# Kernel optimization log

Hardware: AMD Instinct MI355X
Metric: run time of the kernel (lower is better)

## Reference

```python
import jax, jax.numpy as jnp
import numpy as np

B, C, F, T, D = 8, 128, 256, 128, 32


def setup_inputs() -> dict:
    key = jax.random.key(0)
    ks = jax.random.split(key, 7)
    x = jax.random.normal(ks[0], (B, C, F, T), jnp.float32)
    # 1x1 Conv2d over the T axis == linear map on T; weights [out, T], bias [out]
    Wk = jax.random.normal(ks[1], (D, T), jnp.float32) * 0.05
    bk = jax.random.normal(ks[2], (D,), jnp.float32) * 0.05
    Wq = jax.random.normal(ks[3], (D, T), jnp.float32) * 0.05
    bq = jax.random.normal(ks[4], (D,), jnp.float32) * 0.05
    Wv = jax.random.normal(ks[5], (T, T), jnp.float32) * 0.05
    bv = jax.random.normal(ks[6], (T,), jnp.float32) * 0.05
    return {"x": x, "Wk": Wk, "bk": bk, "Wq": Wq, "bq": bq, "Wv": Wv, "bv": bv}


def _proj(xp, W, b):
    # xp: [B, C2, F, T]; W: [out, T] -> [B, F, out, C2]
    return jnp.einsum('bcft,dt->bfdc', xp, W) + b[None, None, :, None]


def reference(x, Wk, bk, Wq, bq, Wv, bv):
    C2 = x.shape[1] // 2
    xr, xi = x[:, :C2], x[:, C2:]
    k_r = _proj(xr, Wk, bk)  # [B,F,D,C2]
    k_i = _proj(xi, Wk, bk)
    q_r = _proj(xr, Wq, bq)
    q_i = _proj(xi, Wq, bq)
    v_r = _proj(xr, Wv, bv)  # [B,F,T,C2]
    v_i = _proj(xi, Wv, bv)
    # complex P = k^H... actually plain k^T q (no conjugate in source)
    P_r = jnp.einsum('bfdc,bfde->bfce', k_r, q_r) - jnp.einsum('bfdc,bfde->bfce', k_i, q_i)
    P_i = jnp.einsum('bfdc,bfde->bfce', k_r, q_i) + jnp.einsum('bfdc,bfde->bfce', k_i, q_r)
    # independent softmaxes over dim=2 (the first C2 axis)
    W_r = jax.nn.softmax(P_r, axis=2)
    W_i = jax.nn.softmax(P_i, axis=2)
    # output = v @ W (complex)
    o_r = jnp.einsum('bftc,bfce->bfte', v_r, W_r) - jnp.einsum('bftc,bfce->bfte', v_i, W_i)
    o_i = jnp.einsum('bftc,bfce->bfte', v_r, W_i) + jnp.einsum('bftc,bfce->bfte', v_i, W_r)
    # permute [B,F,T,C2] -> [B,C2,F,T], concat real/imag on channel axis
    o_r = jnp.transpose(o_r, (0, 3, 1, 2))
    o_i = jnp.transpose(o_i, (0, 3, 1, 2))
    return jnp.concatenate([o_r, o_i], axis=1)  # [B,C,F,T]
```

## Files before the change

kernel.cpp:

```cpp
#include <hip/hip_runtime.h>

typedef __attribute__((ext_vector_type(8))) __bf16 bf16x8;
typedef __attribute__((ext_vector_type(8))) unsigned short ushort8;
typedef __attribute__((ext_vector_type(4))) unsigned short ushort4v;
typedef __attribute__((ext_vector_type(4))) float f32x4;

namespace {
constexpr int kB = 8, kC = 128, kF = 256, kT = 128;

__device__ __forceinline__ int addrXT(int t, int p) { return t * 128 + (p ^ ((t & 7) << 3)); }
__device__ __forceinline__ int addrU(int ri, int e, int s) { return ri * 8192 + e * 128 + (s ^ ((e & 7) << 3)); }
__device__ __forceinline__ int addrK(int m, int c, int p) { return 16384 + m * 2048 + c * 32 + (p ^ ((c & 3) << 3)); }

__device__ __forceinline__ unsigned short b16(float f) {
    __bf16 h = (__bf16)f;
    return __builtin_bit_cast(unsigned short, h);
}

__device__ __forceinline__ bf16x8 ldfrag(const unsigned short* lds, int idx) {
    return __builtin_bit_cast(bf16x8, *(const ushort8*)(lds + idx));
}

__device__ __forceinline__ bf16x8 fneg(bf16x8 a) {
    ushort8 u = __builtin_bit_cast(ushort8, a);
    u ^= (unsigned short)0x8000;
    return __builtin_bit_cast(bf16x8, u);
}

__device__ __forceinline__ bf16x8 fragWg(const float* p) {
    f32x4 a = *(const f32x4*)p;
    f32x4 c = *(const f32x4*)(p + 4);
    bf16x8 r;
    r[0] = (__bf16)a[0]; r[1] = (__bf16)a[1]; r[2] = (__bf16)a[2]; r[3] = (__bf16)a[3];
    r[4] = (__bf16)c[0]; r[5] = (__bf16)c[1]; r[6] = (__bf16)c[2]; r[7] = (__bf16)c[3];
    return r;
}
}

__global__ __launch_bounds__(256, 4)
void chanattn_mfma2(const float* __restrict__ x,
                    const float* __restrict__ Wk, const float* __restrict__ bk,
                    const float* __restrict__ Wq, const float* __restrict__ bq,
                    const float* __restrict__ Wv, const float* __restrict__ bv,
                    float* __restrict__ out)
{
    __shared__ __align__(16) unsigned short lds[20480];

    const int f = blockIdx.x, b = blockIdx.y;
    const int tid = threadIdx.x;
    const int lane = tid & 63;
    const int w = tid >> 6;
    const int lr = lane & 15;
    const int lg = lane >> 4;
    const size_t cstr = (size_t)kF * kT;
    const float* xb = x + ((size_t)b * kC * kF + f) * kT;

    bf16x8 bqr, bqi;
    {
        bf16x8 xr_f[4], xi_f[4];
        #pragma unroll
        for (int ks = 0; ks < 4; ++ks) {
            xr_f[ks] = fragWg(xb + (size_t)(16 * w + lr) * cstr + ks * 32 + 8 * lg);
            xi_f[ks] = fragWg(xb + (size_t)(64 + 16 * w + lr) * cstr + ks * 32 + 8 * lg);
        }
        f32x4 qacc[2][2], kacc[2][2];
        #pragma unroll
        for (int ri = 0; ri < 2; ++ri)
            #pragma unroll
            for (int dt = 0; dt < 2; ++dt) {
                qacc[ri][dt] = (f32x4){0.f, 0.f, 0.f, 0.f};
                kacc[ri][dt] = (f32x4){0.f, 0.f, 0.f, 0.f};
            }
        #pragma unroll
        for (int dt = 0; dt < 2; ++dt)
            #pragma unroll
            for (int ks = 0; ks < 4; ++ks) {
                bf16x8 wq = fragWg(Wq + (size_t)(16 * dt + lr) * kT + ks * 32 + 8 * lg);
                bf16x8 wk = fragWg(Wk + (size_t)(16 * dt + lr) * kT + ks * 32 + 8 * lg);
                qacc[0][dt] = __builtin_amdgcn_mfma_f32_16x16x32_bf16(wq, xr_f[ks], qacc[0][dt], 0, 0, 0);
                qacc[1][dt] = __builtin_amdgcn_mfma_f32_16x16x32_bf16(wq, xi_f[ks], qacc[1][dt], 0, 0, 0);
                kacc[0][dt] = __builtin_amdgcn_mfma_f32_16x16x32_bf16(xr_f[ks], wk, kacc[0][dt], 0, 0, 0);
                kacc[1][dt] = __builtin_amdgcn_mfma_f32_16x16x32_bf16(xi_f[ks], wk, kacc[1][dt], 0, 0, 0);
            }
        const float bk0 = bk[lr], bk1 = bk[16 + lr];
        #pragma unroll
        for (int dt = 0; dt < 2; ++dt) {
            const int pcol = 8 * ((lr >> 2) & 3) + 4 * dt + (lr & 3);
            const float bb = dt ? bk1 : bk0;
            #pragma unroll
            for (int r = 0; r < 4; ++r) {
                const int c = 16 * w + 4 * lg + r;
                lds[addrK(0, c, pcol)] = b16(kacc[0][dt][r] + bb);
                lds[addrK(1, c, pcol)] = b16(kacc[1][dt][r] + bb);
            }
        }
        #pragma unroll
        for (int j = 0; j < 8; ++j) {
            const int dt = j >> 2, r = j & 3;
            const float bb = bq[16 * dt + 4 * lg + r];
            bqr[j] = (__bf16)(qacc[0][dt][r] + bb);
            bqi[j] = (__bf16)(qacc[1][dt][r] + bb);
        }
    }

    {
        const int c0 = 4 * (tid & 31);
        const int t0 = 4 * (tid >> 5);
        const int h  = c0 >> 6;
        const int cc = c0 & 63;
        const int p0 = 64 * h + 32 * (cc >> 5) + 8 * ((cc >> 2) & 3) + 4 * ((cc >> 4) & 1);
        #pragma unroll
        for (int tp = 0; tp < 4; ++tp) {
            const int t = t0 + 32 * tp;
            f32x4 v[4];
            #pragma unroll
            for (int j = 0; j < 4; ++j)
                v[j] = *(const f32x4*)(xb + (size_t)(c0 + j) * cstr + t);
            #pragma unroll
            for (int i = 0; i < 4; ++i) {
                ushort4v pk;
                pk[0] = b16(v[0][i]); pk[1] = b16(v[1][i]);
                pk[2] = b16(v[2][i]); pk[3] = b16(v[3][i]);
                *(ushort4v*)&lds[addrXT(t + i, p0)] = pk;
            }
        }
    }
    __syncthreads();

    f32x4 pr[4], pi[4];
    float inv_r, inv_i;
    {
        const f32x4 zero = {0.f, 0.f, 0.f, 0.f};
        #pragma unroll
        for (int ct = 0; ct < 4; ++ct) {
            bf16x8 akr = ldfrag(lds, addrK(0, ct * 16 + lr, 8 * lg));
            bf16x8 aki = ldfrag(lds, addrK(1, ct * 16 + lr, 8 * lg));
            pr[ct] = __builtin_amdgcn_mfma_f32_16x16x32_bf16(akr, bqr, zero, 0, 0, 0);
            pr[ct] = __builtin_amdgcn_mfma_f32_16x16x32_bf16(fneg(aki), bqi, pr[ct], 0, 0, 0);
            pi[ct] = __builtin_amdgcn_mfma_f32_16x16x32_bf16(akr, bqi, zero, 0, 0, 0);
            pi[ct] = __builtin_amdgcn_mfma_f32_16x16x32_bf16(aki, bqr, pi[ct], 0, 0, 0);
        }
        float mr = -1e30f, mi = -1e30f;
        #pragma unroll
        for (int ct = 0; ct < 4; ++ct)
            #pragma unroll
            for (int r = 0; r < 4; ++r) { mr = fmaxf(mr, pr[ct][r]); mi = fmaxf(mi, pi[ct][r]); }
        mr = fmaxf(mr, __shfl_xor(mr, 16)); mr = fmaxf(mr, __shfl_xor(mr, 32));
        mi = fmaxf(mi, __shfl_xor(mi, 16)); mi = fmaxf(mi, __shfl_xor(mi, 32));
        float sr = 0.f, si = 0.f;
        #pragma unroll
        for (int ct = 0; ct < 4; ++ct)
            #pragma unroll
            for (int r = 0; r < 4; ++r) {
                float er = __expf(pr[ct][r] - mr); pr[ct][r] = er; sr += er;
                float ei = __expf(pi[ct][r] - mi); pi[ct][r] = ei; si += ei;
            }
        sr += __shfl_xor(sr, 16); sr += __shfl_xor(sr, 32);
        si += __shfl_xor(si, 16); si += __shfl_xor(si, 32);
        inv_r = 1.f / sr; inv_i = 1.f / si;
    }

    bf16x8 awr[2], awi[2], awin[2];
    #pragma unroll
    for (int ks = 0; ks < 2; ++ks) {
        #pragma unroll
        for (int j = 0; j < 8; ++j) {
            const int ct = 2 * ks + (j >> 2), r = j & 3;
            awr[ks][j] = (__bf16)(pr[ct][r] * inv_r);
            awi[ks][j] = (__bf16)(pi[ct][r] * inv_i);
        }
        awin[ks] = fneg(awi[ks]);
    }

    f32x4 uacc_r[8], uacc_i[8];
    #pragma unroll
    for (int nt = 0; nt < 8; ++nt) {
        f32x4 ur = {0.f, 0.f, 0.f, 0.f}, ui = {0.f, 0.f, 0.f, 0.f};
        #pragma unroll
        for (int ks = 0; ks < 2; ++ks) {
            bf16x8 bxr = ldfrag(lds, addrXT(nt * 16 + lr, ks * 32 + 8 * lg));
            bf16x8 bxi = ldfrag(lds, addrXT(nt * 16 + lr, 64 + ks * 32 + 8 * lg));
            ur = __builtin_amdgcn_mfma_f32_16x16x32_bf16(awr[ks], bxr, ur, 0, 0, 0);
            ur = __builtin_amdgcn_mfma_f32_16x16x32_bf16(awin[ks], bxi, ur, 0, 0, 0);
            ui = __builtin_amdgcn_mfma_f32_16x16x32_bf16(awi[ks], bxr, ui, 0, 0, 0);
            ui = __builtin_amdgcn_mfma_f32_16x16x32_bf16(awr[ks], bxi, ui, 0, 0, 0);
        }
        uacc_r[nt] = ur; uacc_i[nt] = ui;
    }
    __syncthreads();
    #pragma unroll
    for (int nt = 0; nt < 8; ++nt)
        #pragma unroll
        for (int r = 0; r < 4; ++r) {
            const int e = 16 * w + 4 * lg + r;
            lds[addrU(0, e, nt * 16 + lr)] = b16(uacc_r[nt][r]);
            lds[addrU(1, e, nt * 16 + lr)] = b16(uacc_i[nt][r]);
        }
    __syncthreads();

    {
        #pragma unroll
        for (int mi_ = 0; mi_ < 2; ++mi_) {
            const int mt = 2 * w + mi_;
            bf16x8 av[4];
            #pragma unroll
            for (int ks = 0; ks < 4; ++ks)
                av[ks] = fragWg(Wv + (size_t)(mt * 16 + lr) * kT + ks * 32 + 8 * lg);
            float bvv[4];
            #pragma unroll
            for (int r = 0; r < 4; ++r) bvv[r] = 2.f * bv[mt * 16 + 4 * lg + r];

            #pragma unroll
            for (int et = 0; et < 4; ++et) {
                f32x4 aor = {0.f, 0.f, 0.f, 0.f}, aoi = {0.f, 0.f, 0.f, 0.f};
                #pragma unroll
                for (int ks = 0; ks < 4; ++ks) {
                    bf16x8 bur = ldfrag(lds, addrU(0, et * 16 + lr, ks * 32 + 8 * lg));
                    bf16x8 bui = ldfrag(lds, addrU(1, et * 16 + lr, ks * 32 + 8 * lg));
                    aor = __builtin_amdgcn_mfma_f32_16x16x32_bf16(av[ks], bur, aor, 0, 0, 0);
                    aoi = __builtin_amdgcn_mfma_f32_16x16x32_bf16(av[ks], bui, aoi, 0, 0, 0);
                }
                const int e = et * 16 + lr;
                const int tp0 = mt * 16 + 4 * lg;
                f32x4 vi;
                #pragma unroll
                for (int r = 0; r < 4; ++r) vi[r] = aoi[r] + bvv[r];
                *(f32x4*)(out + (((size_t)b * kC + e) * kF + f) * kT + tp0)      = aor;
                *(f32x4*)(out + (((size_t)b * kC + 64 + e) * kF + f) * kT + tp0) = vi;
            }
        }
    }
}

extern "C" void kernel_launch(void* const* d_in, const int* in_sizes, int n_in,
                              void* d_out, int out_size, void* d_ws, size_t ws_size,
                              hipStream_t stream) {
    const float* x  = (const float*)d_in[0];
    const float* Wk = (const float*)d_in[1];
    const float* bk = (const float*)d_in[2];
    const float* Wq = (const float*)d_in[3];
    const float* bq = (const float*)d_in[4];
    const float* Wv = (const float*)d_in[5];
    const float* bv = (const float*)d_in[6];
    float* out = (float*)d_out;

    dim3 grid(kF, kB);
    dim3 block(256);
    chanattn_mfma2<<<grid, block, 0, stream>>>(x, Wk, bk, Wq, bq, Wv, bv, out);
}
```

Before: 97.59 us.

## Process two frequency bins per block with register prefetch of next x tile

Each block now handles two consecutive f values in a loop, and the grid is halved. The x tile is loaded in halves into registers and the next bin's first half is prefetched while the current bin is being staged, so global load latency overlaps compute. The Q/K projection now reloads its x fragments inside the ks loop instead of holding them all at once, which lowers register pressure. In exchange the grid has fewer blocks, which may cut occupancy and parallelism, and an extra barrier is added per iteration.

```diff
diff --git a/kernel.cpp b/kernel.cpp
--- a/kernel.cpp
+++ b/kernel.cpp
@@ -17,8 +17,8 @@
     return __builtin_bit_cast(unsigned short, h);
 }
 
-__device__ __forceinline__ bf16x8 ldfrag(const unsigned short* lds, int idx) {
-    return __builtin_bit_cast(bf16x8, *(const ushort8*)(lds + idx));
+__device__ __forceinline__ bf16x8 ldfrag(const unsigned short* p, int idx) {
+    return __builtin_bit_cast(bf16x8, *(const ushort8*)(p + idx));
 }
 
 __device__ __forceinline__ bf16x8 fneg(bf16x8 a) {
@@ -38,197 +38,231 @@
 }
 
 __global__ __launch_bounds__(256, 4)
-void chanattn_mfma2(const float* __restrict__ x,
-                    const float* __restrict__ Wk, const float* __restrict__ bk,
-                    const float* __restrict__ Wq, const float* __restrict__ bq,
-                    const float* __restrict__ Wv, const float* __restrict__ bv,
-                    float* __restrict__ out)
+void chanattn_pipe(const float* __restrict__ x,
+                   const float* __restrict__ Wk, const float* __restrict__ bk,
+                   const float* __restrict__ Wq, const float* __restrict__ bq,
+                   const float* __restrict__ Wv, const float* __restrict__ bv,
+                   float* __restrict__ out)
 {
     __shared__ __align__(16) unsigned short lds[20480];
 
-    const int f = blockIdx.x, b = blockIdx.y;
+    const int bx = blockIdx.x, b = blockIdx.y;
     const int tid = threadIdx.x;
     const int lane = tid & 63;
     const int w = tid >> 6;
     const int lr = lane & 15;
     const int lg = lane >> 4;
     const size_t cstr = (size_t)kF * kT;
-    const float* xb = x + ((size_t)b * kC * kF + f) * kT;
-
-    bf16x8 bqr, bqi;
-    {
-        bf16x8 xr_f[4], xi_f[4];
-        #pragma unroll
-        for (int ks = 0; ks < 4; ++ks) {
-            xr_f[ks] = fragWg(xb + (size_t)(16 * w + lr) * cstr + ks * 32 + 8 * lg);
-            xi_f[ks] = fragWg(xb + (size_t)(64 + 16 * w + lr) * cstr + ks * 32 + 8 * lg);
-        }
-        f32x4 qacc[2][2], kacc[2][2];
-        #pragma unroll
-        for (int ri = 0; ri < 2; ++ri)
-            #pragma unroll
-            for (int dt = 0; dt < 2; ++dt) {
-                qacc[ri][dt] = (f32x4){0.f, 0.f, 0.f, 0.f};
-                kacc[ri][dt] = (f32x4){0.f, 0.f, 0.f, 0.f};
-            }
-        #pragma unroll
-        for (int dt = 0; dt < 2; ++dt)
-            #pragma unroll
-            for (int ks = 0; ks < 4; ++ks) {
-                bf16x8 wq = fragWg(Wq + (size_t)(16 * dt + lr) * kT + ks * 32 + 8 * lg);
-                bf16x8 wk = fragWg(Wk + (size_t)(16 * dt + lr) * kT + ks * 32 + 8 * lg);
-                qacc[0][dt] = __builtin_amdgcn_mfma_f32_16x16x32_bf16(wq, xr_f[ks], qacc[0][dt], 0, 0, 0);
-                qacc[1][dt] = __builtin_amdgcn_mfma_f32_16x16x32_bf16(wq, xi_f[ks], qacc[1][dt], 0, 0, 0);
-                kacc[0][dt] = __builtin_amdgcn_mfma_f32_16x16x32_bf16(xr_f[ks], wk, kacc[0][dt], 0, 0, 0);
-                kacc[1][dt] = __builtin_amdgcn_mfma_f32_16x16x32_bf16(xi_f[ks], wk, kacc[1][dt], 0, 0, 0);
-            }
-        const float bk0 = bk[lr], bk1 = bk[16 + lr];
-        #pragma unroll
-        for (int dt = 0; dt < 2; ++dt) {
-            const int pcol = 8 * ((lr >> 2) & 3) + 4 * dt + (lr & 3);
-            const float bb = dt ? bk1 : bk0;
-            #pragma unroll
-            for (int r = 0; r < 4; ++r) {
-                const int c = 16 * w + 4 * lg + r;
-                lds[addrK(0, c, pcol)] = b16(kacc[0][dt][r] + bb);
-                lds[addrK(1, c, pcol)] = b16(kacc[1][dt][r] + bb);
-            }
-        }
-        #pragma unroll
-        for (int j = 0; j < 8; ++j) {
-            const int dt = j >> 2, r = j & 3;
-            const float bb = bq[16 * dt + 4 * lg + r];
-            bqr[j] = (__bf16)(qacc[0][dt][r] + bb);
-            bqi[j] = (__bf16)(qacc[1][dt][r] + bb);
-        }
-    }
-
-    {
-        const int c0 = 4 * (tid & 31);
-        const int t0 = 4 * (tid >> 5);
-        const int h  = c0 >> 6;
-        const int cc = c0 & 63;
-        const int p0 = 64 * h + 32 * (cc >> 5) + 8 * ((cc >> 2) & 3) + 4 * ((cc >> 4) & 1);
-        #pragma unroll
-        for (int tp = 0; tp < 4; ++tp) {
+
+    const int c0 = 4 * (tid & 31);
+    const int t0 = 4 * (tid >> 5);
+    const int h  = c0 >> 6;
+    const int cc = c0 & 63;
+    const int p0 = 64 * h + 32 * (cc >> 5) + 8 * ((cc >> 2) & 3) + 4 * ((cc >> 4) & 1);
+
+    const float* xb_base = x + ((size_t)b * kC * kF + 2 * bx) * kT;
+
+    f32x4 ph0[2][4], ph1[2][4];
+    #pragma unroll
+    for (int tp = 0; tp < 2; ++tp)
+        #pragma unroll
+        for (int j = 0; j < 4; ++j)
+            ph0[tp][j] = *(const f32x4*)(xb_base + (size_t)(c0 + j) * cstr + t0 + 32 * tp);
+
+    #pragma unroll 1
+    for (int n = 0; n < 2; ++n) {
+        const int f = 2 * bx + n;
+        const float* xb = x + ((size_t)b * kC * kF + f) * kT;
+
+        #pragma unroll
+        for (int tp = 0; tp < 2; ++tp)
+            #pragma unroll
+            for (int j = 0; j < 4; ++j)
+                ph1[tp][j] = *(const f32x4*)(xb + (size_t)(c0 + j) * cstr + t0 + 64 + 32 * tp);
+
+        #pragma unroll
+        for (int tp = 0; tp < 2; ++tp) {
             const int t = t0 + 32 * tp;
-            f32x4 v[4];
-            #pragma unroll
-            for (int j = 0; j < 4; ++j)
-                v[j] = *(const f32x4*)(xb + (size_t)(c0 + j) * cstr + t);
             #pragma unroll
             for (int i = 0; i < 4; ++i) {
                 ushort4v pk;
-                pk[0] = b16(v[0][i]); pk[1] = b16(v[1][i]);
-                pk[2] = b16(v[2][i]); pk[3] = b16(v[3][i]);
+                pk[0] = b16(ph0[tp][0][i]); pk[1] = b16(ph0[tp][1][i]);
+                pk[2] = b16(ph0[tp][2][i]); pk[3] = b16(ph0[tp][3][i]);
                 *(ushort4v*)&lds[addrXT(t + i, p0)] = pk;
             }
         }
-    }
-    __syncthreads();
-
-    f32x4 pr[4], pi[4];
-    float inv_r, inv_i;
-    {
-        const f32x4 zero = {0.f, 0.f, 0.f, 0.f};
-        #pragma unroll
-        for (int ct = 0; ct < 4; ++ct) {
-            bf16x8 akr = ldfrag(lds, addrK(0, ct * 16 + lr, 8 * lg));
-            bf16x8 aki = ldfrag(lds, addrK(1, ct * 16 + lr, 8 * lg));
-            pr[ct] = __builtin_amdgcn_mfma_f32_16x16x32_bf16(akr, bqr, zero, 0, 0, 0);
-            pr[ct] = __builtin_amdgcn_mfma_f32_16x16x32_bf16(fneg(aki), bqi, pr[ct], 0, 0, 0);
-            pi[ct] = __builtin_amdgcn_mfma_f32_16x16x32_bf16(akr, bqi, zero, 0, 0, 0);
-            pi[ct] = __builtin_amdgcn_mfma_f32_16x16x32_bf16(aki, bqr, pi[ct], 0, 0, 0);
-        }
-        float mr = -1e30f, mi = -1e30f;
-        #pragma unroll
-        for (int ct = 0; ct < 4; ++ct)
-            #pragma unroll
-            for (int r = 0; r < 4; ++r) { mr = fmaxf(mr, pr[ct][r]); mi = fmaxf(mi, pi[ct][r]); }
-        mr = fmaxf(mr, __shfl_xor(mr, 16)); mr = fmaxf(mr, __shfl_xor(mr, 32));
-        mi = fmaxf(mi, __shfl_xor(mi, 16)); mi = fmaxf(mi, __shfl_xor(mi, 32));
-        float sr = 0.f, si = 0.f;
-        #pragma unroll
-        for (int ct = 0; ct < 4; ++ct)
+
+        if (n == 0) {
+            const float* xb1 = xb_base + kT;
+            #pragma unroll
+            for (int tp = 0; tp < 2; ++tp)
+                #pragma unroll
+                for (int j = 0; j < 4; ++j)
+                    ph0[tp][j] = *(const f32x4*)(xb1 + (size_t)(c0 + j) * cstr + t0 + 32 * tp);
+        }
+
+        #pragma unroll
+        for (int tp = 0; tp < 2; ++tp) {
+            const int t = t0 + 64 + 32 * tp;
+            #pragma unroll
+            for (int i = 0; i < 4; ++i) {
+                ushort4v pk;
+                pk[0] = b16(ph1[tp][0][i]); pk[1] = b16(ph1[tp][1][i]);
+                pk[2] = b16(ph1[tp][2][i]); pk[3] = b16(ph1[tp][3][i]);
+                *(ushort4v*)&lds[addrXT(t + i, p0)] = pk;
+            }
+        }
+
+        bf16x8 bqr, bqi;
+        {
+            f32x4 qacc[2][2], kacc[2][2];
+            #pragma unroll
+            for (int ri = 0; ri < 2; ++ri)
+                #pragma unroll
+                for (int dt = 0; dt < 2; ++dt) {
+                    qacc[ri][dt] = (f32x4){0.f, 0.f, 0.f, 0.f};
+                    kacc[ri][dt] = (f32x4){0.f, 0.f, 0.f, 0.f};
+                }
+            #pragma unroll
+            for (int ks = 0; ks < 4; ++ks) {
+                bf16x8 xr_f = fragWg(xb + (size_t)(16 * w + lr) * cstr + ks * 32 + 8 * lg);
+                bf16x8 xi_f = fragWg(xb + (size_t)(64 + 16 * w + lr) * cstr + ks * 32 + 8 * lg);
+                #pragma unroll
+                for (int dt = 0; dt < 2; ++dt) {
+                    bf16x8 wq = fragWg(Wq + (size_t)(16 * dt + lr) * kT + ks * 32 + 8 * lg);
+                    bf16x8 wk = fragWg(Wk + (size_t)(16 * dt + lr) * kT + ks * 32 + 8 * lg);
+                    qacc[0][dt] = __builtin_amdgcn_mfma_f32_16x16x32_bf16(wq, xr_f, qacc[0][dt], 0, 0, 0);
+                    qacc[1][dt] = __builtin_amdgcn_mfma_f32_16x16x32_bf16(wq, xi_f, qacc[1][dt], 0, 0, 0);
+                    kacc[0][dt] = __builtin_amdgcn_mfma_f32_16x16x32_bf16(xr_f, wk, kacc[0][dt], 0, 0, 0);
+                    kacc[1][dt] = __builtin_amdgcn_mfma_f32_16x16x32_bf16(xi_f, wk, kacc[1][dt], 0, 0, 0);
+                }
+            }
+            const float bk0 = bk[lr], bk1 = bk[16 + lr];
+            #pragma unroll
+            for (int dt = 0; dt < 2; ++dt) {
+                const int pcol = 8 * ((lr >> 2) & 3) + 4 * dt + (lr & 3);
+                const float bb = dt ? bk1 : bk0;
+                #pragma unroll
+                for (int r = 0; r < 4; ++r) {
+                    const int c = 16 * w + 4 * lg + r;
+                    lds[addrK(0, c, pcol)] = b16(kacc[0][dt][r] + bb);
+                    lds[addrK(1, c, pcol)] = b16(kacc[1][dt][r] + bb);
+                }
+            }
+            #pragma unroll
+            for (int j = 0; j < 8; ++j) {
+                const int dt = j >> 2, r = j & 3;
+                const float bb = bq[16 * dt + 4 * lg + r];
+                bqr[j] = (__bf16)(qacc[0][dt][r] + bb);
+                bqi[j] = (__bf16)(qacc[1][dt][r] + bb);
+            }
+        }
+        __syncthreads();
+
+        f32x4 pr[4], pi[4];
+        float inv_r, inv_i;
+        {
+            const f32x4 zero = {0.f, 0.f, 0.f, 0.f};
+            #pragma unroll
+            for (int ct = 0; ct < 4; ++ct) {
+                bf16x8 akr = ldfrag(lds, addrK(0, ct * 16 + lr, 8 * lg));
+                bf16x8 aki = ldfrag(lds, addrK(1, ct * 16 + lr, 8 * lg));
+                pr[ct] = __builtin_amdgcn_mfma_f32_16x16x32_bf16(akr, bqr, zero, 0, 0, 0);
+                pr[ct] = __builtin_amdgcn_mfma_f32_16x16x32_bf16(fneg(aki), bqi, pr[ct], 0, 0, 0);
+                pi[ct] = __builtin_amdgcn_mfma_f32_16x16x32_bf16(akr, bqi, zero, 0, 0, 0);
+                pi[ct] = __builtin_amdgcn_mfma_f32_16x16x32_bf16(aki, bqr, pi[ct], 0, 0, 0);
+            }
+            float mr = -1e30f, mi = -1e30f;
+            #pragma unroll
+            for (int ct = 0; ct < 4; ++ct)
+                #pragma unroll
+                for (int r = 0; r < 4; ++r) { mr = fmaxf(mr, pr[ct][r]); mi = fmaxf(mi, pi[ct][r]); }
+            mr = fmaxf(mr, __shfl_xor(mr, 16)); mr = fmaxf(mr, __shfl_xor(mr, 32));
+            mi = fmaxf(mi, __shfl_xor(mi, 16)); mi = fmaxf(mi, __shfl_xor(mi, 32));
+            float sr = 0.f, si = 0.f;
+            #pragma unroll
+            for (int ct = 0; ct < 4; ++ct)
+                #pragma unroll
+                for (int r = 0; r < 4; ++r) {
+                    float er = __expf(pr[ct][r] - mr); pr[ct][r] = er; sr += er;
+                    float ei = __expf(pi[ct][r] - mi); pi[ct][r] = ei; si += ei;
+                }
+            sr += __shfl_xor(sr, 16); sr += __shfl_xor(sr, 32);
+            si += __shfl_xor(si, 16); si += __shfl_xor(si, 32);
+            inv_r = 1.f / sr; inv_i = 1.f / si;
+        }
+
+        bf16x8 awr[2], awi[2], awin[2];
+        #pragma unroll
+        for (int ks = 0; ks < 2; ++ks) {
+            #pragma unroll
+            for (int j = 0; j < 8; ++j) {
+                const int ct = 2 * ks + (j >> 2), r = j & 3;
+                awr[ks][j] = (__bf16)(pr[ct][r] * inv_r);
+                awi[ks][j] = (__bf16)(pi[ct][r] * inv_i);
+            }
+            awin[ks] = fneg(awi[ks]);
+        }
+
+        f32x4 uacc_r[8], uacc_i[8];
+        #pragma unroll
+        for (int nt = 0; nt < 8; ++nt) {
+            f32x4 ur = {0.f, 0.f, 0.f, 0.f}, ui = {0.f, 0.f, 0.f, 0.f};
+            #pragma unroll
+            for (int ks = 0; ks < 2; ++ks) {
+                bf16x8 bxr = ldfrag(lds, addrXT(nt * 16 + lr, ks * 32 + 8 * lg));
+                bf16x8 bxi = ldfrag(lds, addrXT(nt * 16 + lr, 64 + ks * 32 + 8 * lg));
+                ur = __builtin_amdgcn_mfma_f32_16x16x32_bf16(awr[ks], bxr, ur, 0, 0, 0);
+                ur = __builtin_amdgcn_mfma_f32_16x16x32_bf16(awin[ks], bxi, ur, 0, 0, 0);
+                ui = __builtin_amdgcn_mfma_f32_16x16x32_bf16(awi[ks], bxr, ui, 0, 0, 0);
+                ui = __builtin_amdgcn_mfma_f32_16x16x32_bf16(awr[ks], bxi, ui, 0, 0, 0);
+            }
+            uacc_r[nt] = ur; uacc_i[nt] = ui;
+        }
+        __syncthreads();
+        #pragma unroll
+        for (int nt = 0; nt < 8; ++nt)
             #pragma unroll
             for (int r = 0; r < 4; ++r) {
-                float er = __expf(pr[ct][r] - mr); pr[ct][r] = er; sr += er;
-                float ei = __expf(pi[ct][r] - mi); pi[ct][r] = ei; si += ei;
-            }
-        sr += __shfl_xor(sr, 16); sr += __shfl_xor(sr, 32);
-        si += __shfl_xor(si, 16); si += __shfl_xor(si, 32);
-        inv_r = 1.f / sr; inv_i = 1.f / si;
-    }
-
-    bf16x8 awr[2], awi[2], awin[2];
-    #pragma unroll
-    for (int ks = 0; ks < 2; ++ks) {
-        #pragma unroll
-        for (int j = 0; j < 8; ++j) {
-            const int ct = 2 * ks + (j >> 2), r = j & 3;
-            awr[ks][j] = (__bf16)(pr[ct][r] * inv_r);
-            awi[ks][j] = (__bf16)(pi[ct][r] * inv_i);
-        }
-        awin[ks] = fneg(awi[ks]);
-    }
-
-    f32x4 uacc_r[8], uacc_i[8];
-    #pragma unroll
-    for (int nt = 0; nt < 8; ++nt) {
-        f32x4 ur = {0.f, 0.f, 0.f, 0.f}, ui = {0.f, 0.f, 0.f, 0.f};
-        #pragma unroll
-        for (int ks = 0; ks < 2; ++ks) {
-            bf16x8 bxr = ldfrag(lds, addrXT(nt * 16 + lr, ks * 32 + 8 * lg));
-            bf16x8 bxi = ldfrag(lds, addrXT(nt * 16 + lr, 64 + ks * 32 + 8 * lg));
-            ur = __builtin_amdgcn_mfma_f32_16x16x32_bf16(awr[ks], bxr, ur, 0, 0, 0);
-            ur = __builtin_amdgcn_mfma_f32_16x16x32_bf16(awin[ks], bxi, ur, 0, 0, 0);
-            ui = __builtin_amdgcn_mfma_f32_16x16x32_bf16(awi[ks], bxr, ui, 0, 0, 0);
-            ui = __builtin_amdgcn_mfma_f32_16x16x32_bf16(awr[ks], bxi, ui, 0, 0, 0);
-        }
-        uacc_r[nt] = ur; uacc_i[nt] = ui;
-    }
-    __syncthreads();
-    #pragma unroll
-    for (int nt = 0; nt < 8; ++nt)
-        #pragma unroll
-        for (int r = 0; r < 4; ++r) {
-            const int e = 16 * w + 4 * lg + r;
-            lds[addrU(0, e, nt * 16 + lr)] = b16(uacc_r[nt][r]);
-            lds[addrU(1, e, nt * 16 + lr)] = b16(uacc_i[nt][r]);
-        }
-    __syncthreads();
-
-    {
-        #pragma unroll
-        for (int mi_ = 0; mi_ < 2; ++mi_) {
-            const int mt = 2 * w + mi_;
-            bf16x8 av[4];
-            #pragma unroll
-            for (int ks = 0; ks < 4; ++ks)
-                av[ks] = fragWg(Wv + (size_t)(mt * 16 + lr) * kT + ks * 32 + 8 * lg);
-            float bvv[4];
-            #pragma unroll
-            for (int r = 0; r < 4; ++r) bvv[r] = 2.f * bv[mt * 16 + 4 * lg + r];
-
-            #pragma unroll
-            for (int et = 0; et < 4; ++et) {
-                f32x4 aor = {0.f, 0.f, 0.f, 0.f}, aoi = {0.f, 0.f, 0.f, 0.f};
-                #pragma unroll
-                for (int ks = 0; ks < 4; ++ks) {
-                    bf16x8 bur = ldfrag(lds, addrU(0, et * 16 + lr, ks * 32 + 8 * lg));
-                    bf16x8 bui = ldfrag(lds, addrU(1, et * 16 + lr, ks * 32 + 8 * lg));
-                    aor = __builtin_amdgcn_mfma_f32_16x16x32_bf16(av[ks], bur, aor, 0, 0, 0);
-                    aoi = __builtin_amdgcn_mfma_f32_16x16x32_bf16(av[ks], bui, aoi, 0, 0, 0);
-                }
-                const int e = et * 16 + lr;
+                const int e = 16 * w + 4 * lg + r;
+                lds[addrU(0, e, nt * 16 + lr)] = b16(uacc_r[nt][r]);
+                lds[addrU(1, e, nt * 16 + lr)] = b16(uacc_i[nt][r]);
+            }
+        __syncthreads();
+
+        {
+            #pragma unroll
+            for (int mi_ = 0; mi_ < 2; ++mi_) {
+                const int mt = 2 * w + mi_;
+                bf16x8 av[4];
+                #pragma unroll
+                for (int ks = 0; ks < 4; ++ks)
+                    av[ks] = fragWg(Wv + (size_t)(16 * mt + lr) * kT + ks * 32 + 8 * lg);
                 const int tp0 = mt * 16 + 4 * lg;
-                f32x4 vi;
-                #pragma unroll
-                for (int r = 0; r < 4; ++r) vi[r] = aoi[r] + bvv[r];
-                *(f32x4*)(out + (((size_t)b * kC + e) * kF + f) * kT + tp0)      = aor;
-                *(f32x4*)(out + (((size_t)b * kC + 64 + e) * kF + f) * kT + tp0) = vi;
-            }
-        }
+                float bvv[4];
+                #pragma unroll
+                for (int r = 0; r < 4; ++r) bvv[r] = 2.f * bv[tp0 + r];
+
+                #pragma unroll
+                for (int et = 0; et < 4; ++et) {
+                    f32x4 aor = {0.f, 0.f, 0.f, 0.f}, aoi = {0.f, 0.f, 0.f, 0.f};
+                    #pragma unroll
+                    for (int ks = 0; ks < 4; ++ks) {
+                        bf16x8 bur = ldfrag(lds, addrU(0, et * 16 + lr, ks * 32 + 8 * lg));
+                        bf16x8 bui = ldfrag(lds, addrU(1, et * 16 + lr, ks * 32 + 8 * lg));
+                        aor = __builtin_amdgcn_mfma_f32_16x16x32_bf16(av[ks], bur, aor, 0, 0, 0);
+                        aoi = __builtin_amdgcn_mfma_f32_16x16x32_bf16(av[ks], bui, aoi, 0, 0, 0);
+                    }
+                    const int e = et * 16 + lr;
+                    f32x4 vi;
+                    #pragma unroll
+                    for (int r = 0; r < 4; ++r) vi[r] = aoi[r] + bvv[r];
+                    *(f32x4*)(out + (((size_t)b * kC + e) * kF + f) * kT + tp0)      = aor;
+                    *(f32x4*)(out + (((size_t)b * kC + 64 + e) * kF + f) * kT + tp0) = vi;
+                }
+            }
+        }
+        __syncthreads();
     }
 }
 
@@ -244,7 +278,7 @@
     const float* bv = (const float*)d_in[6];
     float* out = (float*)d_out;
 
-    dim3 grid(kF, kB);
+    dim3 grid(kF / 2, kB);
     dim3 block(256);
-    chanattn_mfma2<<<grid, block, 0, stream>>>(x, Wk, bk, Wq, bq, Wv, bv, out);
-}
+    chanattn_pipe<<<grid, block, 0, stream>>>(x, Wk, bk, Wq, bq, Wv, bv, out);
+}
```

Result: slower. 312.9 us (+220.6%).
